# Kernel tuning notes

Hardware: AMD Instinct MI355X
Metric: run time of the kernel (lower is better)

Reference implementation:

```python
import jax, jax.numpy as jnp
import numpy as np

B, H, W = 8, 56, 56
DIM = 384
NH = 8
HD = DIM // NH          # 48, also the depthwise-conv channel count
WS = 14
HID = 4 * DIM           # mlp hidden
EPS = 1e-5              # torch nn.LayerNorm default
SCALE = HD ** -0.5


def ln(x, w, b):
    m = jnp.mean(x, axis=-1, keepdims=True)
    v = jnp.var(x, axis=-1, keepdims=True)
    return (x - m) * jax.lax.rsqrt(v + EPS) * w + b


def dwconv3x3(x, w):
    # x: [N,H,W,C], w: [3,3,1,C] depthwise (groups=C), stride 1, pad 1, no bias
    return jax.lax.conv_general_dilated(
        x, w, window_strides=(1, 1), padding=((1, 1), (1, 1)),
        dimension_numbers=('NHWC', 'HWIO', 'NHWC'),
        feature_group_count=x.shape[-1])


def rel_table(rel_pos, size):
    # rel_pos: [2*size-1, HD] -> [size, size, HD] via relative coords (stride 1, q==k size)
    idx = jnp.arange(size)[:, None] - jnp.arange(size)[None, :] + (size - 1)
    return rel_pos[idx]


def win_part(x, ws):
    # [N,H,W,C] -> [N*nWh*nWw, ws, ws, C]  (H,W divisible by ws here)
    N, Hh, Ww, C = x.shape
    x = x.reshape(N, Hh // ws, ws, Ww // ws, ws, C)
    return x.transpose(0, 1, 3, 2, 4, 5).reshape(-1, ws, ws, C)


def win_unpart(x, ws, Hh, Ww):
    nW = (Hh // ws) * (Ww // ws)
    N = x.shape[0] // nW
    x = x.reshape(N, Hh // ws, Ww // ws, ws, ws, -1)
    return x.transpose(0, 1, 3, 2, 4, 5).reshape(N, Hh, Ww, -1)


def _forward(x1, x2, norm1_w, norm1_b, qkv_w, qkv_b,
             poolq_w, poolk_w, poolv_w,
             nq_w, nq_b, nk_w, nk_b, nv_w, nv_b,
             rel_h, rel_w, proj_w, proj_b,
             norm2_w, norm2_b, fc1_w, fc1_b, fc2_w, fc2_b):
    # ---- F(x1): MultiScaleAttention(norm1(x1)) ----
    xn = ln(x1, norm1_w, norm1_b)
    qkv = (xn @ qkv_w + qkv_b).reshape(B, H, W, 3, NH, HD)
    qkv = qkv.transpose(3, 0, 4, 1, 2, 5).reshape(3, B * NH, H, W, HD)
    q = ln(dwconv3x3(qkv[0], poolq_w), nq_w, nq_b)
    k = ln(dwconv3x3(qkv[1], poolk_w), nk_w, nk_b)
    v = ln(dwconv3x3(qkv[2], poolv_w), nv_w, nv_b)
    ori_q = q
    qw = win_part(q, WS).reshape(-1, WS * WS, HD)   # [Bw, 196, 48]
    kw = win_part(k, WS).reshape(-1, WS * WS, HD)
    vw = win_part(v, WS).reshape(-1, WS * WS, HD)
    attn = jnp.einsum('bqc,bkc->bqk', qw * SCALE, kw)
    # decomposed relative position bias
    Rh = rel_table(rel_h, WS)                       # [14,14,48]
    Rw = rel_table(rel_w, WS)
    rq = qw.reshape(-1, WS, WS, HD)
    bh = jnp.einsum('bhwc,hkc->bhwk', rq, Rh)
    bw = jnp.einsum('bhwc,wkc->bhwk', rq, Rw)
    attn = (attn.reshape(-1, WS, WS, WS, WS)
            + bh[:, :, :, :, None] + bw[:, :, :, None, :]).reshape(-1, WS * WS, WS * WS)
    attn = jax.nn.softmax(attn, axis=-1)
    o = jnp.einsum('bqk,bkc->bqc', attn, vw).reshape(-1, WS, WS, HD)
    o = win_unpart(o, WS, H, W)
    o = o + ori_q                                    # residual pooling
    o = o.reshape(B, NH, H, W, HD).transpose(0, 2, 3, 1, 4).reshape(B, H, W, DIM)
    f = o @ proj_w + proj_b
    y1 = x1 + f
    # ---- G(y1): Mlp(norm2(y1)) ----
    yn = ln(y1, norm2_w, norm2_b)
    g = jax.nn.gelu(yn @ fc1_w + fc1_b, approximate=False) @ fc2_w + fc2_b
    y2 = x2 + g
    return y1, y2


def setup_inputs() -> dict:
    key = jax.random.key(0)
    ks = jax.random.split(key, 32)
    p = lambda i, shape, s: jax.random.normal(ks[i], shape, jnp.float32) * s
    return {
        'x1': jax.random.normal(ks[0], (B, H, W, DIM), jnp.float32),
        'x2': jax.random.normal(ks[1], (B, H, W, DIM), jnp.float32),
        'norm1_w': jnp.ones((DIM,), jnp.float32),
        'norm1_b': jnp.zeros((DIM,), jnp.float32),
        'qkv_w': p(2, (DIM, 3 * DIM), 0.02),
        'qkv_b': jnp.zeros((3 * DIM,), jnp.float32),
        'poolq_w': p(3, (3, 3, 1, HD), 0.1),
        'poolk_w': p(4, (3, 3, 1, HD), 0.1),
        'poolv_w': p(5, (3, 3, 1, HD), 0.1),
        'nq_w': jnp.ones((HD,), jnp.float32), 'nq_b': jnp.zeros((HD,), jnp.float32),
        'nk_w': jnp.ones((HD,), jnp.float32), 'nk_b': jnp.zeros((HD,), jnp.float32),
        'nv_w': jnp.ones((HD,), jnp.float32), 'nv_b': jnp.zeros((HD,), jnp.float32),
        'rel_h': p(6, (2 * WS - 1, HD), 0.02),
        'rel_w': p(7, (2 * WS - 1, HD), 0.02),
        'proj_w': p(8, (DIM, DIM), 0.02),
        'proj_b': jnp.zeros((DIM,), jnp.float32),
        'norm2_w': jnp.ones((DIM,), jnp.float32),
        'norm2_b': jnp.zeros((DIM,), jnp.float32),
        'fc1_w': p(9, (DIM, HID), 0.02),
        'fc1_b': jnp.zeros((HID,), jnp.float32),
        'fc2_w': p(10, (HID, DIM), 0.02),
        'fc2_b': jnp.zeros((DIM,), jnp.float32),
    }


def reference(x1, x2, norm1_w, norm1_b, qkv_w, qkv_b,
              poolq_w, poolk_w, poolv_w,
              nq_w, nq_b, nk_w, nk_b, nv_w, nv_b,
              rel_h, rel_w, proj_w, proj_b,
              norm2_w, norm2_b, fc1_w, fc1_b, fc2_w, fc2_b):
    return _forward(x1, x2, norm1_w, norm1_b, qkv_w, qkv_b,
                    poolq_w, poolk_w, poolv_w,
                    nq_w, nq_b, nk_w, nk_b, nv_w, nv_b,
                    rel_h, rel_w, proj_w, proj_b,
                    norm2_w, norm2_b, fc1_w, fc1_b, fc2_w, fc2_b)
```

## Files before the change

kernel.cpp:

```cpp
#include <hip/hip_runtime.h>
#include <hip/hip_bf16.h>

typedef unsigned short u16;
typedef unsigned int u32;

#define DEVI __device__ __forceinline__

constexpr int BB = 8, HHc = 56, WWc = 56, DIMC = 384, NHC = 8, HDC = 48, WSZ = 14;
constexpr int NTOK = BB * HHc * WWc;
constexpr int HIDC = 4 * DIMC;
constexpr float EPSF = 1e-5f;
constexpr float SCALEF = 0.14433756729740643f;

typedef short bf16x8 __attribute__((ext_vector_type(8)));
typedef float f32x4 __attribute__((ext_vector_type(4)));

DEVI float b2f(u16 u) { u32 x = ((u32)u) << 16; float f; __builtin_memcpy(&f, &x, 4); return f; }
DEVI float uasf(u32 x) { float f; __builtin_memcpy(&f, &x, 4); return f; }
DEVI u16 f2b(float f) {
  u32 x; __builtin_memcpy(&x, &f, 4);
  u32 r = (x >> 16) & 1u; x += 0x7fffu + r;
  return (u16)(x >> 16);
}

DEVI float wred_sum(float v) {
  #pragma unroll
  for (int o = 32; o; o >>= 1) v += __shfl_xor(v, o);
  return v;
}

#define GLOAD_LDS16(g, l) __builtin_amdgcn_global_load_lds( \
    (const __attribute__((address_space(1))) u32*)(g), \
    (__attribute__((address_space(3))) u32*)(l), 16, 0, 0)

__global__ __launch_bounds__(256)
void wcvt_kernel(const float* __restrict__ in, u16* __restrict__ out, int K, int N) {
  __shared__ float t[32][33];
  int bk = blockIdx.x * 32, bn = blockIdx.y * 32;
  int tx = threadIdx.x & 31, ty = threadIdx.x >> 5;
  #pragma unroll
  for (int i = 0; i < 32; i += 8)
    t[ty + i][tx] = in[(size_t)(bk + ty + i) * N + bn + tx];
  __syncthreads();
  #pragma unroll
  for (int i = 0; i < 32; i += 8)
    out[(size_t)(bn + ty + i) * K + bk + tx] = f2b(t[tx][ty + i]);
}

__global__ __launch_bounds__(256)
void ln384_kernel(const float* __restrict__ x, const float* __restrict__ w,
                  const float* __restrict__ b, u16* __restrict__ out) {
  int wave = threadIdx.x >> 6, lane = threadIdx.x & 63;
  int tok = blockIdx.x * 4 + wave;
  if (tok >= NTOK) return;
  const float* xr = x + (size_t)tok * DIMC;
  float v[6]; float s = 0.f, ss = 0.f;
  #pragma unroll
  for (int i = 0; i < 6; ++i) {
    v[i] = xr[lane + i * 64];
    s += v[i]; ss += v[i] * v[i];
  }
  s = wred_sum(s); ss = wred_sum(ss);
  float mean = s * (1.f / 384.f);
  float var = ss * (1.f / 384.f) - mean * mean;
  float inv = rsqrtf(var + EPSF);
  #pragma unroll
  for (int i = 0; i < 6; ++i) {
    int c = lane + i * 64;
    out[(size_t)(c >> 5) * (NTOK * 32) + (size_t)tok * 32 + (c & 31)] =
        f2b((v[i] - mean) * inv * w[c] + b[c]);
  }
}

template<int MODE, int BN>
__global__ __launch_bounds__(256)
void mgemm_kernel(const u16* __restrict__ A, const u16* __restrict__ Wt,
                  const float* __restrict__ bias, const float* __restrict__ res,
                  void* __restrict__ outv, int M, int N, int K) {
  constexpr int FN = BN / 32;
  __shared__ __attribute__((aligned(16))) u16 As[2][128 * 32];
  __shared__ __attribute__((aligned(16))) u16 Bs[2][BN * 32];
  int tid = threadIdx.x;
  int wave = tid >> 6, lane = tid & 63;
  int wr = wave >> 1, wc = wave & 1;
  int bm0 = blockIdx.x * 128, bn0 = blockIdx.y * BN;
  int lrow = lane >> 2;
  int slot = (lane & 3) ^ ((lane >> 3) & 3);
  const size_t slab = (size_t)M * 32;
  const u16* ag0 = A + (size_t)(bm0 + wave * 32 + lrow) * 32 + slot * 8;
  const u16* ag1 = ag0 + 16 * 32;
  const u16* bg0 = Wt + (size_t)(bn0 + wave * (BN / 4) + lrow) * K + slot * 8;
  const u16* bg1 = bg0 + (size_t)16 * K;
  int q4 = lane >> 4, r16 = lane & 15;
  int rslot = (q4 ^ ((r16 >> 1) & 3)) * 8;
  int aoff = (wr * 64 + r16) * 32 + rslot;
  int boff = (wc * (BN / 2) + r16) * 32 + rslot;
  f32x4 acc[4][FN] = {};
  int nk = K >> 5;
  {
    u16* a0 = As[0] + wave * 1024;
    u16* b0 = Bs[0] + wave * (BN / 4) * 32;
    GLOAD_LDS16(ag0, a0);  GLOAD_LDS16(ag1, a0 + 512);
    GLOAD_LDS16(bg0, b0);
    if constexpr (BN == 128) GLOAD_LDS16(bg1, b0 + 512);
  }
  int cur = 0;
  for (int t = 0; t < nk; ++t) {
    if (t + 1 < nk) {
      int k0 = (t + 1) << 5;
      u16* a0 = As[cur ^ 1] + wave * 1024;
      u16* b0 = Bs[cur ^ 1] + wave * (BN / 4) * 32;
      GLOAD_LDS16(ag0 + (size_t)(t + 1) * slab, a0);
      GLOAD_LDS16(ag1 + (size_t)(t + 1) * slab, a0 + 512);
      GLOAD_LDS16(bg0 + k0, b0);
      if constexpr (BN == 128) GLOAD_LDS16(bg1 + k0, b0 + 512);
      if constexpr (BN == 128) asm volatile("s_waitcnt vmcnt(4)" ::: "memory");
      else                     asm volatile("s_waitcnt vmcnt(3)" ::: "memory");
    } else {
      asm volatile("s_waitcnt vmcnt(0)" ::: "memory");
    }
    __builtin_amdgcn_s_barrier();
    const u16* ar = As[cur] + aoff;
    const u16* br = Bs[cur] + boff;
    bf16x8 af[4], bf[FN];
    #pragma unroll
    for (int f = 0; f < 4; ++f)
      af[f] = *reinterpret_cast<const bf16x8*>(ar + f * 512);
    #pragma unroll
    for (int f = 0; f < FN; ++f)
      bf[f] = *reinterpret_cast<const bf16x8*>(br + f * 512);
    #pragma unroll
    for (int fm = 0; fm < 4; ++fm)
      #pragma unroll
      for (int fn = 0; fn < FN; ++fn)
        acc[fm][fn] = __builtin_amdgcn_mfma_f32_16x16x32_bf16(af[fm], bf[fn], acc[fm][fn], 0, 0, 0);
    asm volatile("s_waitcnt lgkmcnt(0)" ::: "memory");
    __builtin_amdgcn_s_barrier();
    cur ^= 1;
  }
  int c0 = bn0 + wc * (BN / 2) + r16;
  int r0 = bm0 + wr * 64 + q4 * 4;
  #pragma unroll
  for (int fm = 0; fm < 4; ++fm) {
    #pragma unroll
    for (int fn = 0; fn < FN; ++fn) {
      int c = c0 + fn * 16;
      float bsv = bias[c];
      #pragma unroll
      for (int j = 0; j < 4; ++j) {
        int r = r0 + fm * 16 + j;
        float v = acc[fm][fn][j] + bsv;
        if constexpr (MODE == 0) {
          u16* out = (u16*)outv;
          int s = c / DIMC; int rem = c - s * DIMC;
          int nh = rem / HDC; int ch = rem - nh * HDC;
          int b = r / 3136; int hw = r - b * 3136;
          out[(((size_t)(s * 64 + b * 8 + nh)) * 3136 + hw) * 48 + ch] = f2b(v);
        } else if constexpr (MODE == 1) {
          float* out = (float*)outv;
          size_t idx = (size_t)r * N + c;
          out[idx] = v + res[idx];
        } else {
          u16* out = (u16*)outv;
          out[(size_t)(c >> 5) * M * 32 + (size_t)r * 32 + (c & 31)] =
              f2b(0.5f * v * (1.0f + erff(v * 0.70710678118654752440f)));
        }
      }
    }
  }
}

__global__ __launch_bounds__(256)
void convln_kernel(const u16* __restrict__ qkv,
                   const float* __restrict__ wq, const float* __restrict__ wk, const float* __restrict__ wv,
                   const float* __restrict__ gq, const float* __restrict__ bq,
                   const float* __restrict__ gk, const float* __restrict__ bk,
                   const float* __restrict__ gv, const float* __restrict__ bv,
                   u16* __restrict__ out) {
  __shared__ __attribute__((aligned(16))) float wsm[432];
  __shared__ __attribute__((aligned(16))) float gsm[48];
  __shared__ __attribute__((aligned(16))) float bsm[48];
  int tid = threadIdx.x;
  int sb = blockIdx.y;
  int s = sb >> 6;
  const float* wgt = (s == 0) ? wq : ((s == 1) ? wk : wv);
  const float* gam = (s == 0) ? gq : ((s == 1) ? gk : gv);
  const float* bet = (s == 0) ? bq : ((s == 1) ? bk : bv);
  for (int i = tid; i < 432; i += 256) wsm[i] = wgt[i];
  if (tid < 48) { gsm[tid] = gam[tid]; bsm[tid] = bet[tid]; }
  __syncthreads();
  int hw = blockIdx.x * 256 + tid;
  if (hw >= 3136) return;
  int h = hw / 56, w = hw - h * 56;
  const u16* img = qkv + (size_t)sb * (3136 * 48);
  float acc[48];
  #pragma unroll
  for (int c = 0; c < 48; ++c) acc[c] = 0.f;
  #pragma unroll
  for (int dy = -1; dy <= 1; ++dy) {
    int hh = h + dy;
    if ((unsigned)hh >= 56u) continue;
    #pragma unroll
    for (int dx = -1; dx <= 1; ++dx) {
      int ww = w + dx;
      if ((unsigned)ww >= 56u) continue;
      const uint4* p = reinterpret_cast<const uint4*>(img + (size_t)(hh * 56 + ww) * 48);
      const float4* wr = reinterpret_cast<const float4*>(wsm + ((dy + 1) * 3 + (dx + 1)) * 48);
      #pragma unroll
      for (int g = 0; g < 6; ++g) {
        uint4 v = p[g];
        float4 w0 = wr[g * 2], w1 = wr[g * 2 + 1];
        acc[g * 8 + 0] += uasf(v.x << 16)          * w0.x;
        acc[g * 8 + 1] += uasf(v.x & 0xFFFF0000u)  * w0.y;
        acc[g * 8 + 2] += uasf(v.y << 16)          * w0.z;
        acc[g * 8 + 3] += uasf(v.y & 0xFFFF0000u)  * w0.w;
        acc[g * 8 + 4] += uasf(v.z << 16)          * w1.x;
        acc[g * 8 + 5] += uasf(v.z & 0xFFFF0000u)  * w1.y;
        acc[g * 8 + 6] += uasf(v.w << 16)          * w1.z;
        acc[g * 8 + 7] += uasf(v.w & 0xFFFF0000u)  * w1.w;
      }
    }
  }
  float sum = 0.f, ssq = 0.f;
  #pragma unroll
  for (int c = 0; c < 48; ++c) { sum += acc[c]; ssq += acc[c] * acc[c]; }
  float mean = sum * (1.f / 48.f);
  float var = ssq * (1.f / 48.f) - mean * mean;
  float inv = rsqrtf(var + EPSF);
  u16* op = out + ((size_t)sb * 3136 + hw) * 48;
  #pragma unroll
  for (int g = 0; g < 6; ++g) {
    const float4 gm0 = *reinterpret_cast<const float4*>(gsm + g * 8);
    const float4 gm1 = *reinterpret_cast<const float4*>(gsm + g * 8 + 4);
    const float4 bt0 = *reinterpret_cast<const float4*>(bsm + g * 8);
    const float4 bt1 = *reinterpret_cast<const float4*>(bsm + g * 8 + 4);
    uint4 ov;
    u32 a0 = f2b((acc[g * 8 + 0] - mean) * inv * gm0.x + bt0.x);
    u32 a1 = f2b((acc[g * 8 + 1] - mean) * inv * gm0.y + bt0.y);
    u32 a2 = f2b((acc[g * 8 + 2] - mean) * inv * gm0.z + bt0.z);
    u32 a3 = f2b((acc[g * 8 + 3] - mean) * inv * gm0.w + bt0.w);
    u32 a4 = f2b((acc[g * 8 + 4] - mean) * inv * gm1.x + bt1.x);
    u32 a5 = f2b((acc[g * 8 + 5] - mean) * inv * gm1.y + bt1.y);
    u32 a6 = f2b((acc[g * 8 + 6] - mean) * inv * gm1.z + bt1.z);
    u32 a7 = f2b((acc[g * 8 + 7] - mean) * inv * gm1.w + bt1.w);
    ov.x = a0 | (a1 << 16);
    ov.y = a2 | (a3 << 16);
    ov.z = a4 | (a5 << 16);
    ov.w = a6 | (a7 << 16);
    *reinterpret_cast<uint4*>(op + g * 8) = ov;
  }
}

#define MFMA16(a, b, c) __builtin_amdgcn_mfma_f32_16x16x32_bf16((a), (b), (c), 0, 0, 0)
constexpr int LDP = 224;
constexpr int LDK = 104;
constexpr int LDV = 228;
__global__ __launch_bounds__(512, 1)
void attn_kernel(const u16* __restrict__ qkvc, const float* __restrict__ rel_h,
                 const float* __restrict__ rel_w, u16* __restrict__ obuf) {
  __shared__ __attribute__((aligned(16))) u16 KL[208 * LDK];
  __shared__ __attribute__((aligned(16))) u16 VT[48 * LDV];
  __shared__ __attribute__((aligned(16))) u16 QE[208 * 56];
  __shared__ __attribute__((aligned(16))) u16 PB[8 * 16 * LDP];

  int wid = blockIdx.x;
  int bnh = wid >> 4, wrem = wid & 15, wh = wrem >> 2, wwn = wrem & 3;
  int tid = threadIdx.x;
  int wave = tid >> 6, lane = tid & 63;
  int q4 = lane >> 4, r16 = lane & 15;

  { u32* z;
    z = (u32*)KL; for (int i = tid; i < 208 * LDK / 2; i += 512) z[i] = 0;
    z = (u32*)VT; for (int i = tid; i < 48 * LDV / 2; i += 512) z[i] = 0;
    z = (u32*)PB; for (int i = tid; i < 64 * 72 / 2; i += 512) z[i] = 0;
  }
  __syncthreads();
  size_t qbase = (size_t)bnh * 3136 * 48;
  size_t kbase = ((size_t)(64 + bnh) * 3136) * 48;
  size_t vbase = ((size_t)(128 + bnh) * 3136) * 48;
  for (int i = tid; i < 196 * 12; i += 512) {
    int r = i / 12, c4 = (i - r * 12) * 4;
    int h = wh * 14 + r / 14, w = wwn * 14 + r % 14;
    size_t g = (size_t)(h * 56 + w) * 48 + c4;
    ushort4 kv = *reinterpret_cast<const ushort4*>(qkvc + kbase + g);
    kv.x = f2b(b2f(kv.x) * SCALEF); kv.y = f2b(b2f(kv.y) * SCALEF);
    kv.z = f2b(b2f(kv.z) * SCALEF); kv.w = f2b(b2f(kv.w) * SCALEF);
    *reinterpret_cast<ushort4*>(KL + r * LDK + c4) = kv;
    ushort4 vv = *reinterpret_cast<const ushort4*>(qkvc + vbase + g);
    VT[(c4 + 0) * LDV + r] = vv.x; VT[(c4 + 1) * LDV + r] = vv.y;
    VT[(c4 + 2) * LDV + r] = vv.z; VT[(c4 + 3) * LDV + r] = vv.w;
  }
  for (int r = tid; r < 208; r += 512) {
    if (r < 196) {
      KL[r * LDK + 48 + r / 14] = 0x3F80;
      KL[r * LDK + 62 + r % 14] = 0x3F80;
    } else {
      KL[r * LDK + 76] = 0x3F80;
    }
  }
  for (int i = tid; i < 54 * 48; i += 512) {
    int r = i / 48, c = i - r * 48;
    float v = (r < 27) ? rel_h[r * 48 + c] : rel_w[(r - 27) * 48 + c];
    PB[r * 72 + c] = f2b(v);
  }
  __syncthreads();
  for (int mf = wave; mf < 13; mf += 8) {
    int qrow = mf * 16 + r16; int qc = qrow < 196 ? qrow : 195;
    int hq = wh * 14 + qc / 14, wq = wwn * 14 + qc % 14;
    const u16* qpg = qkvc + qbase + (size_t)(hq * 56 + wq) * 48;
    bf16x8 af0 = *reinterpret_cast<const bf16x8*>(qpg + q4 * 8);
    bf16x8 af1 = {0, 0, 0, 0, 0, 0, 0, 0};
    if (q4 < 2) af1 = *reinterpret_cast<const bf16x8*>(qpg + 32 + q4 * 8);
    #pragma unroll
    for (int nf = 0; nf < 4; ++nf) {
      bf16x8 b0 = *reinterpret_cast<const bf16x8*>(PB + (nf * 16 + r16) * 72 + q4 * 8);
      bf16x8 b1 = *reinterpret_cast<const bf16x8*>(PB + (nf * 16 + r16) * 72 + 32 + q4 * 8);
      f32x4 acc = {};
      acc = MFMA16(af0, b0, acc);
      acc = MFMA16(af1, b1, acc);
      int col = nf * 16 + r16;
      if (col < 54) {
        #pragma unroll
        for (int j = 0; j < 4; ++j)
          QE[(mf * 16 + q4 * 4 + j) * 56 + col] = f2b(acc[j]);
      }
    }
  }
  __syncthreads();
  u16 bhv[14], bwv[14];
  {
    int t = tid;
    if (t < 208) {
      int qc = t < 196 ? t : 195;
      int qh = qc / 14, qw = qc - qh * 14;
      const u16* src = QE + t * 56;
      #pragma unroll
      for (int z = 0; z < 14; ++z) {
        bhv[z] = src[qh + 13 - z];
        bwv[z] = src[27 + qw + 13 - z];
      }
    }
  }
  __syncthreads();
  {
    int t = tid;
    if (t < 208) {
      u16* dst = QE + t * 56;
      #pragma unroll
      for (int z = 0; z < 14; ++z) { dst[z] = bhv[z]; dst[14 + z] = bwv[z]; }
      dst[28] = f2b(-30000.0f);
      #pragma unroll
      for (int z = 29; z < 56; ++z) dst[z] = 0;
    }
  }
  u16* Pw = PB + wave * 16 * LDP;
  for (int i = lane; i < 16 * 16; i += 64) {
    int r = i >> 4;
    Pw[r * LDP + ((208 + (i & 15)) ^ (((r >> 2) & 3) << 3))] = 0;
  }
  __syncthreads();
  int bI = bnh >> 3, nhI = bnh & 7;
  for (int mf = wave; mf < 13; mf += 8) {
    int qrow = mf * 16 + r16; int qc = qrow < 196 ? qrow : 195;
    int hq = wh * 14 + qc / 14, wq = wwn * 14 + qc % 14;
    const u16* qpg = qkvc + qbase + (size_t)(hq * 56 + wq) * 48;
    const u16* qe = QE + qrow * 56;
    bf16x8 af0 = *reinterpret_cast<const bf16x8*>(qpg + q4 * 8);
    bf16x8 af1;
    if (q4 < 2) af1 = *reinterpret_cast<const bf16x8*>(qpg + 32 + q4 * 8);
    else        af1 = *reinterpret_cast<const bf16x8*>(qe + (q4 - 2) * 8);
    bf16x8 af2 = *reinterpret_cast<const bf16x8*>(qe + 16 + q4 * 8);
    f32x4 s[13];
    #pragma unroll
    for (int nf = 0; nf < 13; ++nf) {
      const u16* kr = KL + (nf * 16 + r16) * LDK;
      bf16x8 b0 = *reinterpret_cast<const bf16x8*>(kr + q4 * 8);
      bf16x8 b1 = *reinterpret_cast<const bf16x8*>(kr + 32 + q4 * 8);
      bf16x8 b2 = *reinterpret_cast<const bf16x8*>(kr + 64 + q4 * 8);
      f32x4 a = {};
      a = MFMA16(af0, b0, a);
      a = MFMA16(af1, b1, a);
      a = MFMA16(af2, b2, a);
      s[nf] = a;
    }
    int rowb = mf * 16 + q4 * 4;
    float mrow[4], den[4];
    #pragma unroll
    for (int j = 0; j < 4; ++j) {
      float mm = s[0][j];
      #pragma unroll
      for (int nf = 1; nf < 13; ++nf) mm = fmaxf(mm, s[nf][j]);
      #pragma unroll
      for (int off = 1; off < 16; off <<= 1) mm = fmaxf(mm, __shfl_xor(mm, off));
      mrow[j] = mm; den[j] = 0.f;
    }
    #pragma unroll
    for (int nf = 0; nf < 13; ++nf) {
      #pragma unroll
      for (int j = 0; j < 4; ++j) {
        float p = __expf(s[nf][j] - mrow[j]);
        den[j] += p;
        Pw[(q4 * 4 + j) * LDP + (((nf * 16 + r16) ^ (q4 << 3)))] = f2b(p);
      }
    }
    #pragma unroll
    for (int j = 0; j < 4; ++j)
      #pragma unroll
      for (int off = 1; off < 16; off <<= 1) den[j] += __shfl_xor(den[j], off);
    f32x4 o[3] = {};
    #pragma unroll
    for (int ks = 0; ks < 7; ++ks) {
      bf16x8 ap = *reinterpret_cast<const bf16x8*>(
          Pw + r16 * LDP + ((ks * 32 + q4 * 8) ^ (((r16 >> 2) & 3) << 3)));
      #pragma unroll
      for (int nf3 = 0; nf3 < 3; ++nf3) {
        bf16x8 bv = *reinterpret_cast<const bf16x8*>(VT + (nf3 * 16 + r16) * LDV + ks * 32 + q4 * 8);
        o[nf3] = MFMA16(ap, bv, o[nf3]);
      }
    }
    #pragma unroll
    for (int j = 0; j < 4; ++j) {
      int row = rowb + j;
      if (row < 196) {
        float rden = 1.f / den[j];
        int rh = row / 14;
        int h = wh * 14 + rh, w = wwn * 14 + row - rh * 14;
        int tok = (bI * 56 + h) * 56 + w;
        const u16* qg = qkvc + qbase + (size_t)(h * 56 + w) * 48;
        #pragma unroll
        for (int nf3 = 0; nf3 < 3; ++nf3) {
          int col = nf3 * 16 + r16;
          int cg = nhI * 48 + col;
          obuf[(size_t)(cg >> 5) * (NTOK * 32) + (size_t)tok * 32 + (cg & 31)] =
              f2b(o[nf3][j] * rden + b2f(qg[col]));
        }
      }
    }
  }
}

extern "C" void kernel_launch(void* const* d_in, const int* in_sizes, int n_in,
                              void* d_out, int out_size, void* d_ws, size_t ws_size,
                              hipStream_t stream) {
  const float* x1      = (const float*)d_in[0];
  const float* x2      = (const float*)d_in[1];
  const float* norm1_w = (const float*)d_in[2];
  const float* norm1_b = (const float*)d_in[3];
  const float* qkv_w   = (const float*)d_in[4];
  const float* qkv_b   = (const float*)d_in[5];
  const float* poolq_w = (const float*)d_in[6];
  const float* poolk_w = (const float*)d_in[7];
  const float* poolv_w = (const float*)d_in[8];
  const float* nq_w    = (const float*)d_in[9];
  const float* nq_b    = (const float*)d_in[10];
  const float* nk_w    = (const float*)d_in[11];
  const float* nk_b    = (const float*)d_in[12];
  const float* nv_w    = (const float*)d_in[13];
  const float* nv_b    = (const float*)d_in[14];
  const float* rel_h   = (const float*)d_in[15];
  const float* rel_w   = (const float*)d_in[16];
  const float* proj_w  = (const float*)d_in[17];
  const float* proj_b  = (const float*)d_in[18];
  const float* norm2_w = (const float*)d_in[19];
  const float* norm2_b = (const float*)d_in[20];
  const float* fc1_w   = (const float*)d_in[21];
  const float* fc1_b   = (const float*)d_in[22];
  const float* fc2_w   = (const float*)d_in[23];
  const float* fc2_b   = (const float*)d_in[24];

  u16* ws      = (u16*)d_ws;
  u16* qkv     = ws;
  u16* xn      = ws + 28901376;
  u16* qkvc    = ws + 28901376;
  u16* obuf    = ws;
  u16* h1      = ws;
  u16* yn      = ws + 48168960;
  u16* qkv_wt  = ws + 38535168;
  u16* proj_wt = ws + 9633792;
  u16* fc1_wt  = ws + 38535168;
  u16* fc2_wt  = ws + 39124992;
  float* y1 = (float*)d_out;
  float* y2 = y1 + 9633792;

  wcvt_kernel<<<dim3(12, 36), 256, 0, stream>>>(qkv_w, qkv_wt, 384, 1152);
  ln384_kernel<<<NTOK / 4, 256, 0, stream>>>(x1, norm1_w, norm1_b, xn);
  mgemm_kernel<0, 128><<<dim3(196, 9), 256, 0, stream>>>(xn, qkv_wt, qkv_b, nullptr, qkv, NTOK, 1152, 384);
  convln_kernel<<<dim3(13, 192), 256, 0, stream>>>(qkv, poolq_w, poolk_w, poolv_w,
                                                   nq_w, nq_b, nk_w, nk_b, nv_w, nv_b, qkvc);
  wcvt_kernel<<<dim3(12, 12), 256, 0, stream>>>(proj_w, proj_wt, 384, 384);
  attn_kernel<<<1024, 512, 0, stream>>>(qkvc, rel_h, rel_w, obuf);
  wcvt_kernel<<<dim3(12, 48), 256, 0, stream>>>(fc1_w, fc1_wt, 384, 1536);
  wcvt_kernel<<<dim3(48, 12), 256, 0, stream>>>(fc2_w, fc2_wt, 1536, 384);
  mgemm_kernel<1, 64><<<dim3(196, 6), 256, 0, stream>>>(obuf, proj_wt, proj_b, x1, y1, NTOK, 384, 384);
  ln384_kernel<<<NTOK / 4, 256, 0, stream>>>(y1, norm2_w, norm2_b, yn);
  mgemm_kernel<2, 128><<<dim3(196, 12), 256, 0, stream>>>(yn, fc1_wt, fc1_b, nullptr, h1, NTOK, 1536, 384);
  mgemm_kernel<1, 64><<<dim3(196, 6), 256, 0, stream>>>(h1, fc2_wt, fc2_b, x2, y2, NTOK, 384, 1536);
}
```

Before: 361.4 us.

## Fuse MLP fc1+GELU+fc2 into one kernel keeping hidden activations in LDS

Replaces the separate fc1 GEMM (writing the GELU'd hidden tensor to global memory) and fc2 GEMM with one kernel per 64-token tile. Each tile computes hidden chunks of 128 columns into shared memory, applies bias and GELU, then accumulates the fc2 product in registers and adds bias and residual. This removes the global round trip of the large hidden activation. The cost is that weight B-fragments are read straight from global/L2 with no LDS staging or double buffering, and there are only 392 blocks, so tiles may be smaller and less latency-hidden than in the tuned GEMM.

```diff
diff --git a/kernel.cpp b/kernel.cpp
--- a/kernel.cpp
+++ b/kernel.cpp
@@ -32,6 +32,8 @@
 #define GLOAD_LDS16(g, l) __builtin_amdgcn_global_load_lds( \
     (const __attribute__((address_space(1))) u32*)(g), \
     (__attribute__((address_space(3))) u32*)(l), 16, 0, 0)
+
+#define MFMA16(a, b, c) __builtin_amdgcn_mfma_f32_16x16x32_bf16((a), (b), (c), 0, 0, 0)
 
 __global__ __launch_bounds__(256)
 void wcvt_kernel(const float* __restrict__ in, u16* __restrict__ out, int K, int N) {
@@ -156,17 +158,99 @@
           int nh = rem / HDC; int ch = rem - nh * HDC;
           int b = r / 3136; int hw = r - b * 3136;
           out[(((size_t)(s * 64 + b * 8 + nh)) * 3136 + hw) * 48 + ch] = f2b(v);
-        } else if constexpr (MODE == 1) {
+        } else {
           float* out = (float*)outv;
           size_t idx = (size_t)r * N + c;
           out[idx] = v + res[idx];
-        } else {
-          u16* out = (u16*)outv;
-          out[(size_t)(c >> 5) * M * 32 + (size_t)r * 32 + (c & 31)] =
-              f2b(0.5f * v * (1.0f + erff(v * 0.70710678118654752440f)));
         }
       }
     }
+  }
+}
+
+constexpr int LDY = 392;
+constexpr int LDH = 136;
+__global__ __launch_bounds__(256, 2)
+void mlp_kernel(const u16* __restrict__ yn, const u16* __restrict__ w1t,
+                const float* __restrict__ b1, const u16* __restrict__ w2t,
+                const float* __restrict__ b2, const float* __restrict__ x2,
+                float* __restrict__ y2) {
+  __shared__ __attribute__((aligned(16))) u16 Ys[64 * LDY];
+  __shared__ __attribute__((aligned(16))) u16 Hs[64 * LDH];
+  int tid = threadIdx.x;
+  int wave = tid >> 6, lane = tid & 63;
+  int q4 = lane >> 4, r16 = lane & 15;
+  int tok0 = blockIdx.x * 64;
+  for (int i = tid; i < 64 * 48; i += 256) {
+    int r = i / 48, g = i - r * 48;
+    int slab = g >> 2, sc = (g & 3) * 8;
+    uint4 v = *reinterpret_cast<const uint4*>(
+        yn + (size_t)slab * (NTOK * 32) + (size_t)(tok0 + r) * 32 + sc);
+    *reinterpret_cast<uint4*>(Ys + r * LDY + g * 8) = v;
+  }
+  f32x4 acc[4][6] = {};
+  int n2w = wave * 96;
+  for (int c = 0; c < 12; ++c) {
+    __syncthreads();
+    int n1w = c * 128 + wave * 32;
+    f32x4 hacc[4][2] = {};
+    #pragma unroll
+    for (int kk = 0; kk < 12; ++kk) {
+      bf16x8 bfr[2];
+      #pragma unroll
+      for (int fn = 0; fn < 2; ++fn)
+        bfr[fn] = *reinterpret_cast<const bf16x8*>(
+            w1t + (size_t)(n1w + fn * 16 + r16) * 384 + kk * 32 + q4 * 8);
+      #pragma unroll
+      for (int fm = 0; fm < 4; ++fm) {
+        bf16x8 af = *reinterpret_cast<const bf16x8*>(
+            Ys + (fm * 16 + r16) * LDY + kk * 32 + q4 * 8);
+        hacc[fm][0] = MFMA16(af, bfr[0], hacc[fm][0]);
+        hacc[fm][1] = MFMA16(af, bfr[1], hacc[fm][1]);
+      }
+    }
+    #pragma unroll
+    for (int fn = 0; fn < 2; ++fn) {
+      int hcol = wave * 32 + fn * 16 + r16;
+      float bb = b1[c * 128 + hcol];
+      #pragma unroll
+      for (int fm = 0; fm < 4; ++fm)
+        #pragma unroll
+        for (int j = 0; j < 4; ++j) {
+          float v = hacc[fm][fn][j] + bb;
+          v = 0.5f * v * (1.0f + erff(v * 0.70710678118654752440f));
+          Hs[(fm * 16 + q4 * 4 + j) * LDH + hcol] = f2b(v);
+        }
+    }
+    __syncthreads();
+    #pragma unroll
+    for (int kk = 0; kk < 4; ++kk) {
+      bf16x8 af[4];
+      #pragma unroll
+      for (int fm = 0; fm < 4; ++fm)
+        af[fm] = *reinterpret_cast<const bf16x8*>(
+            Hs + (fm * 16 + r16) * LDH + kk * 32 + q4 * 8);
+      #pragma unroll
+      for (int fn = 0; fn < 6; ++fn) {
+        bf16x8 bfr = *reinterpret_cast<const bf16x8*>(
+            w2t + (size_t)(n2w + fn * 16 + r16) * 1536 + c * 128 + kk * 32 + q4 * 8);
+        #pragma unroll
+        for (int fm = 0; fm < 4; ++fm)
+          acc[fm][fn] = MFMA16(af[fm], bfr, acc[fm][fn]);
+      }
+    }
+  }
+  #pragma unroll
+  for (int fn = 0; fn < 6; ++fn) {
+    int cgl = n2w + fn * 16 + r16;
+    float bb = b2[cgl];
+    #pragma unroll
+    for (int fm = 0; fm < 4; ++fm)
+      #pragma unroll
+      for (int j = 0; j < 4; ++j) {
+        size_t idx = (size_t)(tok0 + fm * 16 + q4 * 4 + j) * 384 + cgl;
+        y2[idx] = acc[fm][fn][j] + bb + x2[idx];
+      }
   }
 }
 
@@ -251,7 +335,6 @@
   }
 }
 
-#define MFMA16(a, b, c) __builtin_amdgcn_mfma_f32_16x16x32_bf16((a), (b), (c), 0, 0, 0)
 constexpr int LDP = 224;
 constexpr int LDK = 104;
 constexpr int LDV = 228;
@@ -473,7 +556,6 @@
   u16* xn      = ws + 28901376;
   u16* qkvc    = ws + 28901376;
   u16* obuf    = ws;
-  u16* h1      = ws;
   u16* yn      = ws + 48168960;
   u16* qkv_wt  = ws + 38535168;
   u16* proj_wt = ws + 9633792;
@@ -493,6 +575,5 @@
   wcvt_kernel<<<dim3(48, 12), 256, 0, stream>>>(fc2_w, fc2_wt, 1536, 384);
   mgemm_kernel<1, 64><<<dim3(196, 6), 256, 0, stream>>>(obuf, proj_wt, proj_b, x1, y1, NTOK, 384, 384);
   ln384_kernel<<<NTOK / 4, 256, 0, stream>>>(y1, norm2_w, norm2_b, yn);
-  mgemm_kernel<2, 128><<<dim3(196, 12), 256, 0, stream>>>(yn, fc1_wt, fc1_b, nullptr, h1, NTOK, 1536, 384);
-  mgemm_kernel<1, 64><<<dim3(196, 6), 256, 0, stream>>>(h1, fc2_wt, fc2_b, x2, y2, NTOK, 384, 1536);
-}
+  mlp_kernel<<<NTOK / 64, 256, 0, stream>>>(yn, fc1_wt, fc1_b, fc2_wt, fc2_b, x2, y2);
+}
```

Result: slower. 394.3 us (+9.1%).
